# Performance work log

Hardware: AMD Instinct MI355X
Metric: run time of the kernel (lower is better)

## Reference

```python
import jax, jax.numpy as jnp
import numpy as np

N_NODES = 100000
N_EDGES = 1600000
F_IN, HID, N_CLS = 512, 256, 40


def setup_inputs() -> dict:
    key = jax.random.key(0)
    k1, k2, k3, k4 = jax.random.split(key, 4)
    features = jax.random.normal(k1, (N_NODES, F_IN), dtype=jnp.float32)
    # Glorot-ish scaled weights
    W1 = jax.random.normal(k2, (F_IN, HID), dtype=jnp.float32) * (1.0 / np.sqrt(F_IN))
    b1 = jnp.zeros((HID,), dtype=jnp.float32)
    W2 = jax.random.normal(k3, (HID, N_CLS), dtype=jnp.float32) * (1.0 / np.sqrt(HID))
    b2 = jnp.zeros((N_CLS,), dtype=jnp.float32)
    edge_index = jax.random.randint(k4, (2, N_EDGES), 0, N_NODES, dtype=jnp.int64)
    return {"features": features, "W1": W1, "b1": b1, "W2": W2, "b2": b2,
            "edge_index": edge_index}


def _gcn_conv(x, W, b, src, dst, n_nodes):
    # PyG GCNConv: h = X W; out = D^{-1/2}(A+I)D^{-1/2} h + b
    h = x @ W  # [N, out]
    # degree with self-loops (in-degree on dst + 1)
    deg = jax.ops.segment_sum(jnp.ones_like(dst, dtype=h.dtype), dst,
                              num_segments=n_nodes) + 1.0
    dinv = jax.lax.rsqrt(deg)  # [N]
    norm = dinv[src] * dinv[dst]  # [E]
    # gather-normalize-scatter over edges, plus self-loop term dinv_i^2 * h_i
    agg = jax.ops.segment_sum(h[src] * norm[:, None], dst, num_segments=n_nodes)
    agg = agg + h * (dinv * dinv)[:, None]
    return agg + b


def reference(features, W1, b1, W2, b2, edge_index):
    src, dst = edge_index[0], edge_index[1]
    n = features.shape[0]
    x = jax.nn.relu(_gcn_conv(features, W1, b1, src, dst, n))
    # dropout is identity in eval mode (training=False)
    x = _gcn_conv(x, W2, b2, src, dst, n)
    return jax.nn.log_softmax(x, axis=1), jax.nn.softmax(x, axis=1)
```

## Files before the change

### kernel.cpp

```cpp
#include <hip/hip_runtime.h>
#include <hip/hip_bf16.h>


#define F_IN 512
#define HID  256
#define NCLS 40
#define NPAD 48

typedef __attribute__((ext_vector_type(8))) short bf16x8;
typedef __attribute__((ext_vector_type(4))) float floatx4;

__device__ inline unsigned short f2bf(float v) {
    unsigned u = __float_as_uint(v);
    u += 0x7fffu + ((u >> 16) & 1u);
    return (unsigned short)(u >> 16);
}
__device__ inline float bf2f(unsigned short u) {
    return __uint_as_float(((unsigned)u) << 16);
}

__global__ void detect64_kernel(const int* __restrict__ ei, int* __restrict__ flag) {
    __shared__ int any_nz;
    if (threadIdx.x == 0) any_nz = 0;
    __syncthreads();
    int nz = 0;
    for (int i = threadIdx.x; i < 4096; i += 256) {
        nz |= (ei[2 * i + 1] != 0);
    }
    if (nz) atomicOr(&any_nz, 1);
    __syncthreads();
    if (threadIdx.x == 0) *flag = any_nz ? 0 : 1;
}

__device__ inline int edge_src(const int* ei, long long E, int e, int is64) {
    return is64 ? ei[2LL * e] : ei[e];
}
__device__ inline int edge_dst(const int* ei, long long E, int e, int is64) {
    return is64 ? ei[2LL * (E + e)] : ei[(int)E + e];
}

__global__ void count_kernel(const int* __restrict__ ei, int E,
                             const int* __restrict__ flag, int* __restrict__ cnt) {
    int e = blockIdx.x * 256 + threadIdx.x;
    if (e >= E) return;
    int is64 = *flag;
    int d = edge_dst(ei, E, e, is64);
    atomicAdd(&cnt[d], 1);
}

__global__ __launch_bounds__(256) void scan_block_sums(const int* __restrict__ cnt,
                                                       int* __restrict__ blockSums, int Nn) {
    __shared__ int sdata[256];
    int b = blockIdx.x, t = threadIdx.x;
    int sum = 0;
    int i0 = b * 1024 + t * 4;
    for (int i = 0; i < 4; ++i) {
        int idx = i0 + i;
        if (idx < Nn) sum += cnt[idx];
    }
    sdata[t] = sum;
    __syncthreads();
    for (int s = 128; s > 0; s >>= 1) {
        if (t < s) sdata[t] += sdata[t + s];
        __syncthreads();
    }
    if (t == 0) blockSums[b] = sdata[0];
}

__global__ void scan_sums_kernel(int* __restrict__ blockSums, int nB,
                                 int* __restrict__ rowStart, int Nn) {
    if (threadIdx.x == 0 && blockIdx.x == 0) {
        int run = 0;
        for (int i = 0; i < nB; ++i) { int v = blockSums[i]; blockSums[i] = run; run += v; }
        rowStart[Nn] = run;
    }
}

__global__ __launch_bounds__(256) void scan_final(const int* __restrict__ cnt,
                                                  const int* __restrict__ blockSumsEx,
                                                  int* __restrict__ rowStart,
                                                  int* __restrict__ rowPos, int Nn) {
    __shared__ int sdata[256];
    int b = blockIdx.x, t = threadIdx.x;
    int base = blockSumsEx[b];
    int vals[4];
    int sum = 0;
    int i0 = b * 1024 + t * 4;
    for (int i = 0; i < 4; ++i) {
        int idx = i0 + i;
        vals[i] = (idx < Nn) ? cnt[idx] : 0;
        sum += vals[i];
    }
    sdata[t] = sum;
    __syncthreads();
    for (int off = 1; off < 256; off <<= 1) {
        int y = (t >= off) ? sdata[t - off] : 0;
        __syncthreads();
        sdata[t] += y;
        __syncthreads();
    }
    int run = base + (sdata[t] - sum);
    for (int i = 0; i < 4; ++i) {
        int idx = i0 + i;
        if (idx < Nn) { rowStart[idx] = run; rowPos[idx] = run; }
        run += vals[i];
    }
}

__global__ void dinv_kernel(const int* __restrict__ cnt, float* __restrict__ dinv, int Nn) {
    int i = blockIdx.x * 256 + threadIdx.x;
    if (i < Nn) dinv[i] = rsqrtf((float)cnt[i] + 1.0f);
}

__global__ void fill_kernel(const int* __restrict__ ei, int E, const int* __restrict__ flag,
                            const float* __restrict__ dinv, int* __restrict__ rowPos,
                            int* __restrict__ csrSrc, float* __restrict__ csrNorm) {
    int e = blockIdx.x * 256 + threadIdx.x;
    if (e >= E) return;
    int is64 = *flag;
    int s = edge_src(ei, E, e, is64);
    int d = edge_dst(ei, E, e, is64);
    int p = atomicAdd(&rowPos[d], 1);
    csrSrc[p] = s;
    csrNorm[p] = dinv[s] * dinv[d];
}

__global__ __launch_bounds__(256) void convertX_kernel(const float* __restrict__ X,
                                                       unsigned short* __restrict__ Xb,
                                                       int realElems, int totElems) {
    int i = (blockIdx.x * 256 + threadIdx.x) * 4;
    if (i >= totElems) return;
    float4 v = make_float4(0.f, 0.f, 0.f, 0.f);
    if (i < realElems) v = *(const float4*)&X[i];
    ushort4 o;
    o.x = f2bf(v.x); o.y = f2bf(v.y); o.z = f2bf(v.z); o.w = f2bf(v.w);
    *(ushort4*)&Xb[i] = o;
}

__global__ __launch_bounds__(256) void convertW1t_kernel(const float* __restrict__ W1,
                                                         unsigned short* __restrict__ W1t) {
    int id = blockIdx.x * 256 + threadIdx.x;
    int k = id >> 8, n = id & 255;
    W1t[n * 512 + k] = f2bf(W1[id]);
}

__global__ __launch_bounds__(256) void convertW2t_kernel(const float* __restrict__ W2,
                                                         unsigned short* __restrict__ W2t) {
    int id = blockIdx.x * 256 + threadIdx.x;
    if (id >= NPAD * HID) return;
    int n = id / HID, k = id % HID;
    W2t[id] = (n < NCLS) ? f2bf(W2[k * NCLS + n]) : (unsigned short)0;
}

#define LDK 40
__global__ __launch_bounds__(256) void gemm1_mfma_kernel(const unsigned short* __restrict__ Xb,
                                                         const unsigned short* __restrict__ W1t,
                                                         unsigned short* __restrict__ h1) {
    __shared__ unsigned short As[128][LDK];
    __shared__ unsigned short Bs[128][LDK];
    const int tid = threadIdx.x;
    const int bm = blockIdx.x * 128;
    const int bn = blockIdx.y * 128;
    const int lane = tid & 63, w = tid >> 6;
    const int mblk = (w & 1) * 64, nblk = (w >> 1) * 64;
    const int lrow = lane & 15, lq = lane >> 4;

    floatx4 acc[4][4];
#pragma unroll
    for (int i = 0; i < 4; ++i)
#pragma unroll
        for (int j = 0; j < 4; ++j)
            acc[i][j] = (floatx4){0.f, 0.f, 0.f, 0.f};

    for (int k0 = 0; k0 < F_IN; k0 += 32) {
#pragma unroll
        for (int i = 0; i < 2; ++i) {
            int c = tid + i * 256;
            int row = c >> 2, kb = (c & 3) * 8;
            *(float4*)&As[row][kb] =
                *(const float4*)&Xb[(size_t)(bm + row) * F_IN + k0 + kb];
            *(float4*)&Bs[row][kb] =
                *(const float4*)&W1t[(size_t)(bn + row) * F_IN + k0 + kb];
        }
        __syncthreads();
        bf16x8 a[4], b[4];
#pragma unroll
        for (int mt = 0; mt < 4; ++mt)
            a[mt] = *(const bf16x8*)&As[mblk + mt * 16 + lrow][lq * 8];
#pragma unroll
        for (int nt = 0; nt < 4; ++nt)
            b[nt] = *(const bf16x8*)&Bs[nblk + nt * 16 + lrow][lq * 8];
#pragma unroll
        for (int mt = 0; mt < 4; ++mt)
#pragma unroll
            for (int nt = 0; nt < 4; ++nt)
                acc[mt][nt] = __builtin_amdgcn_mfma_f32_16x16x32_bf16(
                    a[mt], b[nt], acc[mt][nt], 0, 0, 0);
        __syncthreads();
    }
#pragma unroll
    for (int mt = 0; mt < 4; ++mt) {
#pragma unroll
        for (int nt = 0; nt < 4; ++nt) {
            int gn = bn + nblk + nt * 16 + lrow;
            size_t gm0 = (size_t)(bm + mblk + mt * 16 + lq * 4);
#pragma unroll
            for (int r = 0; r < 4; ++r)
                h1[(gm0 + r) * HID + gn] = f2bf(acc[mt][nt][r]);
        }
    }
}

__global__ __launch_bounds__(256) void agg1_kernel(const unsigned short* __restrict__ h1,
                                                   const int* __restrict__ rowStart,
                                                   const int* __restrict__ csrSrc,
                                                   const float* __restrict__ csrNorm,
                                                   const float* __restrict__ dinv,
                                                   const float* __restrict__ b1,
                                                   unsigned short* __restrict__ x1b, int Nn) {
    int n = blockIdx.x * 4 + (threadIdx.x >> 6);
    int lane = threadIdx.x & 63;
    if (n >= Nn) return;
    float4 acc = make_float4(0.f, 0.f, 0.f, 0.f);
    int s0 = rowStart[n], s1 = rowStart[n + 1];
    for (int e = s0; e < s1; ++e) {
        int s = csrSrc[e];
        float nrm = csrNorm[e];
        ushort4 v = *(const ushort4*)(h1 + (size_t)s * HID + lane * 4);
        acc.x += nrm * bf2f(v.x);
        acc.y += nrm * bf2f(v.y);
        acc.z += nrm * bf2f(v.z);
        acc.w += nrm * bf2f(v.w);
    }
    float di = dinv[n];
    float self = di * di;
    ushort4 hv = *(const ushort4*)(h1 + (size_t)n * HID + lane * 4);
    float4 bv = *(const float4*)(b1 + lane * 4);
    ushort4 o;
    o.x = f2bf(fmaxf(acc.x + self * bf2f(hv.x) + bv.x, 0.f));
    o.y = f2bf(fmaxf(acc.y + self * bf2f(hv.y) + bv.y, 0.f));
    o.z = f2bf(fmaxf(acc.z + self * bf2f(hv.z) + bv.z, 0.f));
    o.w = f2bf(fmaxf(acc.w + self * bf2f(hv.w) + bv.w, 0.f));
    *(ushort4*)(x1b + (size_t)n * HID + lane * 4) = o;
}

__global__ __launch_bounds__(256) void gemm2_mfma_kernel(const unsigned short* __restrict__ x1b,
                                                         const unsigned short* __restrict__ W2t,
                                                         float* __restrict__ h2, int Nn) {
    const int tid = threadIdx.x;
    const int lane = tid & 63, w = tid >> 6;
    const int base = blockIdx.x * 128 + w * 32;
    const int lrow = lane & 15, lq = lane >> 4;

    floatx4 acc[2][3];
#pragma unroll
    for (int i = 0; i < 2; ++i)
#pragma unroll
        for (int j = 0; j < 3; ++j)
            acc[i][j] = (floatx4){0.f, 0.f, 0.f, 0.f};

#pragma unroll
    for (int k0 = 0; k0 < HID; k0 += 32) {
        bf16x8 a[2], b[3];
#pragma unroll
        for (int mt = 0; mt < 2; ++mt)
            a[mt] = *(const bf16x8*)&x1b[(size_t)(base + mt * 16 + lrow) * HID + k0 + lq * 8];
#pragma unroll
        for (int nt = 0; nt < 3; ++nt)
            b[nt] = *(const bf16x8*)&W2t[(size_t)(nt * 16 + lrow) * HID + k0 + lq * 8];
#pragma unroll
        for (int mt = 0; mt < 2; ++mt)
#pragma unroll
            for (int nt = 0; nt < 3; ++nt)
                acc[mt][nt] = __builtin_amdgcn_mfma_f32_16x16x32_bf16(
                    a[mt], b[nt], acc[mt][nt], 0, 0, 0);
    }
#pragma unroll
    for (int mt = 0; mt < 2; ++mt) {
#pragma unroll
        for (int nt = 0; nt < 3; ++nt) {
            int gn = nt * 16 + lrow;
            int gm0 = base + mt * 16 + lq * 4;
            if (gn < NCLS) {
#pragma unroll
                for (int r = 0; r < 4; ++r) {
                    int gm = gm0 + r;
                    if (gm < Nn) h2[(size_t)gm * NCLS + gn] = acc[mt][nt][r];
                }
            }
        }
    }
}

__global__ __launch_bounds__(256) void agg2_kernel(const float* __restrict__ h2,
                                                   const int* __restrict__ rowStart,
                                                   const int* __restrict__ csrSrc,
                                                   const float* __restrict__ csrNorm,
                                                   const float* __restrict__ dinv,
                                                   const float* __restrict__ b2,
                                                   float* __restrict__ out, int Nn) {
    int n = blockIdx.x * 4 + (threadIdx.x >> 6);
    int lane = threadIdx.x & 63;
    if (n >= Nn) return;
    bool act = lane < NCLS;
    float acc = 0.f;
    int s0 = rowStart[n], s1 = rowStart[n + 1];
    for (int e = s0; e < s1; ++e) {
        int s = csrSrc[e];
        float nrm = csrNorm[e];
        if (act) acc += nrm * h2[(size_t)s * NCLS + lane];
    }
    float di = dinv[n];
    if (act) acc += di * di * h2[(size_t)n * NCLS + lane] + b2[lane];
    float v = act ? acc : -3.4e38f;
#pragma unroll
    for (int off = 32; off > 0; off >>= 1) v = fmaxf(v, __shfl_xor(v, off));
    float ex = act ? expf(acc - v) : 0.f;
    float ssum = ex;
#pragma unroll
    for (int off = 32; off > 0; off >>= 1) ssum += __shfl_xor(ssum, off);
    if (act) {
        float ls = acc - v - logf(ssum);
        out[(size_t)n * NCLS + lane] = ls;
        out[(size_t)Nn * NCLS + (size_t)n * NCLS + lane] = ex / ssum;
    }
}

extern "C" void kernel_launch(void* const* d_in, const int* in_sizes, int n_in,
                              void* d_out, int out_size, void* d_ws, size_t ws_size,
                              hipStream_t stream) {
    const float* features = (const float*)d_in[0];
    const float* W1 = (const float*)d_in[1];
    const float* b1 = (const float*)d_in[2];
    const float* W2 = (const float*)d_in[3];
    const float* b2 = (const float*)d_in[4];
    const int* edge_index = (const int*)d_in[5];

    const int N = in_sizes[0] / F_IN;
    const int E = in_sizes[5] / 2;
    const int Mpad = (N + 127) & ~127;
    float* out = (float*)d_out;

    auto align256 = [](size_t x) { return (x + 255) & ~(size_t)255; };
    char* w = (char*)d_ws;
    int* cnt        = (int*)w;  w += align256((size_t)N * 4);
    int* rowStart   = (int*)w;  w += align256((size_t)(N + 1) * 4);
    int* rowPos     = (int*)w;  w += align256((size_t)N * 4);
    int* blockSums  = (int*)w;  w += align256(1024 * 4);
    int* flag64     = (int*)w;  w += 256;
    int* csrSrc     = (int*)w;  w += align256((size_t)E * 4);
    float* csrNorm  = (float*)w; w += align256((size_t)E * 4);
    float* dinv     = (float*)w; w += align256((size_t)N * 4);
    unsigned short* Xb  = (unsigned short*)w; w += align256((size_t)Mpad * F_IN * 2);
    unsigned short* W1t = (unsigned short*)w; w += align256((size_t)HID * F_IN * 2);
    unsigned short* W2t = (unsigned short*)w; w += align256((size_t)NPAD * HID * 2);
    unsigned short* h1  = (unsigned short*)w; w += align256((size_t)Mpad * HID * 2);
    unsigned short* x1b = (unsigned short*)w; w += align256((size_t)Mpad * HID * 2);
    float* h2       = (float*)w; w += align256((size_t)N * NCLS * 4);
    (void)ws_size;

    const int nB = (N + 1023) / 1024;
    const int eBlocks = (E + 255) / 256;
    const int nBlocks = (N + 255) / 256;
    const int waveBlocks = (N + 3) / 4;

    hipMemsetAsync(cnt, 0, (size_t)N * 4, stream);
    detect64_kernel<<<1, 256, 0, stream>>>(edge_index, flag64);
    count_kernel<<<eBlocks, 256, 0, stream>>>(edge_index, E, flag64, cnt);
    scan_block_sums<<<nB, 256, 0, stream>>>(cnt, blockSums, N);
    scan_sums_kernel<<<1, 64, 0, stream>>>(blockSums, nB, rowStart, N);
    dinv_kernel<<<nBlocks, 256, 0, stream>>>(cnt, dinv, N);
    scan_final<<<nB, 256, 0, stream>>>(cnt, blockSums, rowStart, rowPos, N);
    fill_kernel<<<eBlocks, 256, 0, stream>>>(edge_index, E, flag64, dinv, rowPos,
                                             csrSrc, csrNorm);

    {
        int tot = Mpad * F_IN, real = N * F_IN;
        convertX_kernel<<<(tot / 4 + 255) / 256, 256, 0, stream>>>(features, Xb, real, tot);
        convertW1t_kernel<<<(F_IN * HID) / 256, 256, 0, stream>>>(W1, W1t);
        convertW2t_kernel<<<(NPAD * HID + 255) / 256, 256, 0, stream>>>(W2, W2t);
    }

    dim3 g1(Mpad / 128, HID / 128);
    gemm1_mfma_kernel<<<g1, 256, 0, stream>>>(Xb, W1t, h1);
    agg1_kernel<<<waveBlocks, 256, 0, stream>>>(h1, rowStart, csrSrc, csrNorm, dinv,
                                                b1, x1b, N);
    gemm2_mfma_kernel<<<Mpad / 128, 256, 0, stream>>>(x1b, W2t, h2, N);
    agg2_kernel<<<waveBlocks, 256, 0, stream>>>(h2, rowStart, csrSrc, csrNorm, dinv,
                                                b2, out, N);
}
```

Baseline: 912.8 us.

## Fuse X bf16 conversion into GEMM1, unroll aggregations, store h2 as bf16

```diff
diff --git a/kernel.cpp b/kernel.cpp
--- a/kernel.cpp
+++ b/kernel.cpp
@@ -125,18 +125,6 @@
     csrNorm[p] = dinv[s] * dinv[d];
 }
 
-__global__ __launch_bounds__(256) void convertX_kernel(const float* __restrict__ X,
-                                                       unsigned short* __restrict__ Xb,
-                                                       int realElems, int totElems) {
-    int i = (blockIdx.x * 256 + threadIdx.x) * 4;
-    if (i >= totElems) return;
-    float4 v = make_float4(0.f, 0.f, 0.f, 0.f);
-    if (i < realElems) v = *(const float4*)&X[i];
-    ushort4 o;
-    o.x = f2bf(v.x); o.y = f2bf(v.y); o.z = f2bf(v.z); o.w = f2bf(v.w);
-    *(ushort4*)&Xb[i] = o;
-}
-
 __global__ __launch_bounds__(256) void convertW1t_kernel(const float* __restrict__ W1,
                                                          unsigned short* __restrict__ W1t) {
     int id = blockIdx.x * 256 + threadIdx.x;
@@ -153,9 +141,9 @@
 }
 
 #define LDK 40
-__global__ __launch_bounds__(256) void gemm1_mfma_kernel(const unsigned short* __restrict__ Xb,
+__global__ __launch_bounds__(256) void gemm1_mfma_kernel(const float* __restrict__ X,
                                                          const unsigned short* __restrict__ W1t,
-                                                         unsigned short* __restrict__ h1) {
+                                                         unsigned short* __restrict__ h1, int Nn) {
     __shared__ unsigned short As[128][LDK];
     __shared__ unsigned short Bs[128][LDK];
     const int tid = threadIdx.x;
@@ -174,11 +162,20 @@
 
     for (int k0 = 0; k0 < F_IN; k0 += 32) {
 #pragma unroll
+        for (int i = 0; i < 4; ++i) {
+            int c = tid + i * 256;
+            int row = c >> 3, kb = (c & 7) * 4;
+            int gm = bm + row;
+            float4 v = make_float4(0.f, 0.f, 0.f, 0.f);
+            if (gm < Nn) v = *(const float4*)&X[(size_t)gm * F_IN + k0 + kb];
+            ushort4 o;
+            o.x = f2bf(v.x); o.y = f2bf(v.y); o.z = f2bf(v.z); o.w = f2bf(v.w);
+            *(ushort4*)&As[row][kb] = o;
+        }
+#pragma unroll
         for (int i = 0; i < 2; ++i) {
             int c = tid + i * 256;
             int row = c >> 2, kb = (c & 3) * 8;
-            *(float4*)&As[row][kb] =
-                *(const float4*)&Xb[(size_t)(bm + row) * F_IN + k0 + kb];
             *(float4*)&Bs[row][kb] =
                 *(const float4*)&W1t[(size_t)(bn + row) * F_IN + k0 + kb];
         }
@@ -223,7 +220,20 @@
     if (n >= Nn) return;
     float4 acc = make_float4(0.f, 0.f, 0.f, 0.f);
     int s0 = rowStart[n], s1 = rowStart[n + 1];
-    for (int e = s0; e < s1; ++e) {
+    int e = s0;
+    for (; e + 3 < s1; e += 4) {
+        int iA = csrSrc[e], iB = csrSrc[e + 1], iC = csrSrc[e + 2], iD = csrSrc[e + 3];
+        float nA = csrNorm[e], nB = csrNorm[e + 1], nC = csrNorm[e + 2], nD = csrNorm[e + 3];
+        ushort4 vA = *(const ushort4*)(h1 + (size_t)iA * HID + lane * 4);
+        ushort4 vB = *(const ushort4*)(h1 + (size_t)iB * HID + lane * 4);
+        ushort4 vC = *(const ushort4*)(h1 + (size_t)iC * HID + lane * 4);
+        ushort4 vD = *(const ushort4*)(h1 + (size_t)iD * HID + lane * 4);
+        acc.x += nA * bf2f(vA.x) + nB * bf2f(vB.x) + nC * bf2f(vC.x) + nD * bf2f(vD.x);
+        acc.y += nA * bf2f(vA.y) + nB * bf2f(vB.y) + nC * bf2f(vC.y) + nD * bf2f(vD.y);
+        acc.z += nA * bf2f(vA.z) + nB * bf2f(vB.z) + nC * bf2f(vC.z) + nD * bf2f(vD.z);
+        acc.w += nA * bf2f(vA.w) + nB * bf2f(vB.w) + nC * bf2f(vC.w) + nD * bf2f(vD.w);
+    }
+    for (; e < s1; ++e) {
         int s = csrSrc[e];
         float nrm = csrNorm[e];
         ushort4 v = *(const ushort4*)(h1 + (size_t)s * HID + lane * 4);
@@ -246,7 +256,7 @@
 
 __global__ __launch_bounds__(256) void gemm2_mfma_kernel(const unsigned short* __restrict__ x1b,
                                                          const unsigned short* __restrict__ W2t,
-                                                         float* __restrict__ h2, int Nn) {
+                                                         unsigned short* __restrict__ h2b) {
     const int tid = threadIdx.x;
     const int lane = tid & 63, w = tid >> 6;
     const int base = blockIdx.x * 128 + w * 32;
@@ -281,18 +291,14 @@
         for (int nt = 0; nt < 3; ++nt) {
             int gn = nt * 16 + lrow;
             int gm0 = base + mt * 16 + lq * 4;
-            if (gn < NCLS) {
-#pragma unroll
-                for (int r = 0; r < 4; ++r) {
-                    int gm = gm0 + r;
-                    if (gm < Nn) h2[(size_t)gm * NCLS + gn] = acc[mt][nt][r];
-                }
-            }
+#pragma unroll
+            for (int r = 0; r < 4; ++r)
+                h2b[(size_t)(gm0 + r) * NPAD + gn] = f2bf(acc[mt][nt][r]);
         }
     }
 }
 
-__global__ __launch_bounds__(256) void agg2_kernel(const float* __restrict__ h2,
+__global__ __launch_bounds__(256) void agg2_kernel(const unsigned short* __restrict__ h2b,
                                                    const int* __restrict__ rowStart,
                                                    const int* __restrict__ csrSrc,
                                                    const float* __restrict__ csrNorm,
@@ -303,15 +309,25 @@
     int lane = threadIdx.x & 63;
     if (n >= Nn) return;
     bool act = lane < NCLS;
+    int cl = act ? lane : 0;
     float acc = 0.f;
     int s0 = rowStart[n], s1 = rowStart[n + 1];
-    for (int e = s0; e < s1; ++e) {
+    int e = s0;
+    for (; e + 3 < s1; e += 4) {
+        int iA = csrSrc[e], iB = csrSrc[e + 1], iC = csrSrc[e + 2], iD = csrSrc[e + 3];
+        float nA = csrNorm[e], nB = csrNorm[e + 1], nC = csrNorm[e + 2], nD = csrNorm[e + 3];
+        float vA = bf2f(h2b[(size_t)iA * NPAD + cl]);
+        float vB = bf2f(h2b[(size_t)iB * NPAD + cl]);
+        float vC = bf2f(h2b[(size_t)iC * NPAD + cl]);
+        float vD = bf2f(h2b[(size_t)iD * NPAD + cl]);
+        acc += nA * vA + nB * vB + nC * vC + nD * vD;
+    }
+    for (; e < s1; ++e) {
         int s = csrSrc[e];
-        float nrm = csrNorm[e];
-        if (act) acc += nrm * h2[(size_t)s * NCLS + lane];
+        acc += csrNorm[e] * bf2f(h2b[(size_t)s * NPAD + cl]);
     }
     float di = dinv[n];
-    if (act) acc += di * di * h2[(size_t)n * NCLS + lane] + b2[lane];
+    acc += di * di * bf2f(h2b[(size_t)n * NPAD + cl]) + b2[cl];
     float v = act ? acc : -3.4e38f;
 #pragma unroll
     for (int off = 32; off > 0; off >>= 1) v = fmaxf(v, __shfl_xor(v, off));
@@ -351,12 +367,11 @@
     int* csrSrc     = (int*)w;  w += align256((size_t)E * 4);
     float* csrNorm  = (float*)w; w += align256((size_t)E * 4);
     float* dinv     = (float*)w; w += align256((size_t)N * 4);
-    unsigned short* Xb  = (unsigned short*)w; w += align256((size_t)Mpad * F_IN * 2);
     unsigned short* W1t = (unsigned short*)w; w += align256((size_t)HID * F_IN * 2);
     unsigned short* W2t = (unsigned short*)w; w += align256((size_t)NPAD * HID * 2);
     unsigned short* h1  = (unsigned short*)w; w += align256((size_t)Mpad * HID * 2);
     unsigned short* x1b = (unsigned short*)w; w += align256((size_t)Mpad * HID * 2);
-    float* h2       = (float*)w; w += align256((size_t)N * NCLS * 4);
+    unsigned short* h2b = (unsigned short*)w; w += align256((size_t)Mpad * NPAD * 2);
     (void)ws_size;
 
     const int nB = (N + 1023) / 1024;
@@ -374,18 +389,14 @@
     fill_kernel<<<eBlocks, 256, 0, stream>>>(edge_index, E, flag64, dinv, rowPos,
                                              csrSrc, csrNorm);
 
-    {
-        int tot = Mpad * F_IN, real = N * F_IN;
-        convertX_kernel<<<(tot / 4 + 255) / 256, 256, 0, stream>>>(features, Xb, real, tot);
-        convertW1t_kernel<<<(F_IN * HID) / 256, 256, 0, stream>>>(W1, W1t);
-        convertW2t_kernel<<<(NPAD * HID + 255) / 256, 256, 0, stream>>>(W2, W2t);
-    }
+    convertW1t_kernel<<<(F_IN * HID) / 256, 256, 0, stream>>>(W1, W1t);
+    convertW2t_kernel<<<(NPAD * HID + 255) / 256, 256, 0, stream>>>(W2, W2t);
 
     dim3 g1(Mpad / 128, HID / 128);
-    gemm1_mfma_kernel<<<g1, 256, 0, stream>>>(Xb, W1t, h1);
+    gemm1_mfma_kernel<<<g1, 256, 0, stream>>>(features, W1t, h1, N);
     agg1_kernel<<<waveBlocks, 256, 0, stream>>>(h1, rowStart, csrSrc, csrNorm, dinv,
                                                 b1, x1b, N);
-    gemm2_mfma_kernel<<<Mpad / 128, 256, 0, stream>>>(x1b, W2t, h2, N);
-    agg2_kernel<<<waveBlocks, 256, 0, stream>>>(h2, rowStart, csrSrc, csrNorm, dinv,
+    gemm2_mfma_kernel<<<Mpad / 128, 256, 0, stream>>>(x1b, W2t, h2b);
+    agg2_kernel<<<waveBlocks, 256, 0, stream>>>(h2b, rowStart, csrSrc, csrNorm, dinv,
                                                 b2, out, N);
 }
```

Result: faster. 786.8 us (-13.8%).
